# Kernel tuning notes

Measured on AMD Instinct MI355X. Metric: run time of the kernel, lower is better.

The kernel has to match this reference:

```python
import jax, jax.numpy as jnp
import numpy as np

V, D = 1_000_000, 128
N0, N1, N2 = 1_048_576, 131_072, 16_384
E0, E1, EP = 1_048_576, 131_072, 16_384


def setup_inputs() -> dict:
    key = jax.random.key(0)
    ks = jax.random.split(key, 20)
    inp = {
        'emb': jax.random.normal(ks[0], (V, D), jnp.float32) * 0.1,
        'bias': jnp.zeros((V, 1), jnp.float32),
        'nids': jax.random.randint(ks[1], (N0,), 0, V),
        'src0': jax.random.randint(ks[2], (E0,), 0, N0),
        'dst0': jax.random.randint(ks[3], (E0,), 0, N1),
        'w0': jax.random.uniform(ks[4], (E0,), jnp.float32),
        'src1': jax.random.randint(ks[5], (E1,), 0, N1),
        'dst1': jax.random.randint(ks[6], (E1,), 0, N2),
        'w1': jax.random.uniform(ks[7], (E1,), jnp.float32),
        'pos_src': jax.random.randint(ks[8], (EP,), 0, N2),
        'pos_dst': jax.random.randint(ks[9], (EP,), 0, N2),
        'neg_src': jax.random.randint(ks[10], (EP,), 0, N2),
        'neg_dst': jax.random.randint(ks[11], (EP,), 0, N2),
        'Q0w': jax.random.normal(ks[12], (D, D), jnp.float32) / np.sqrt(D),
        'Q0b': jnp.zeros((D,), jnp.float32),
        'W0w': jax.random.normal(ks[13], (2 * D, D), jnp.float32) / np.sqrt(2 * D),
        'W0b': jnp.zeros((D,), jnp.float32),
        'Q1w': jax.random.normal(ks[14], (D, D), jnp.float32) / np.sqrt(D),
        'Q1b': jnp.zeros((D,), jnp.float32),
        'W1w': jax.random.normal(ks[15], (2 * D, D), jnp.float32) / np.sqrt(2 * D),
        'W1b': jnp.zeros((D,), jnp.float32),
    }
    return inp


def _sage_conv(h_src, h_dst, src, dst, w, Qw, Qb, Ww, Wb, n_dst):
    # n = relu(Q h_src); m = sum_e w_e * n[src_e] per dst; ws = sum_e w_e per dst
    n = jax.nn.relu(h_src @ Qw + Qb)                                   # [N_src, H]
    m = jax.ops.segment_sum(n[src] * w[:, None], dst, num_segments=n_dst)
    ws = jnp.clip(jax.ops.segment_sum(w, dst, num_segments=n_dst), 1.0, None)[:, None]
    z = jax.nn.relu(jnp.concatenate([m / ws, h_dst], axis=1) @ Ww + Wb)
    zn = jnp.linalg.norm(z, axis=1, keepdims=True)
    return z / jnp.where(zn == 0, 1.0, zn)


def _pair_score(h, bias_nid, src, dst):
    # u_dot_v + bias_src + bias_dst  -> [E, 1]
    s = jnp.sum(h[src] * h[dst], axis=1, keepdims=True)
    return s + bias_nid[src] + bias_nid[dst]


def reference(emb, bias, nids, src0, dst0, w0, src1, dst1, w1,
              pos_src, pos_dst, neg_src, neg_dst,
              Q0w, Q0b, W0w, W0b, Q1w, Q1b, W1w, W1b):
    h = emb[nids]                                                      # [N0, D]
    h1 = _sage_conv(h, h[:N1], src0, dst0, w0, Q0w, Q0b, W0w, W0b, N1)  # [N1, D]
    h2 = _sage_conv(h1, h1[:N2], src1, dst1, w1, Q1w, Q1b, W1w, W1b, N2)  # [N2, D]
    h_item = emb[nids[:N2]] + h2                                       # [N2, D]
    bias_nid = bias[nids[:N2]]                                         # [N2, 1]
    pos = _pair_score(h_item, bias_nid, pos_src, pos_dst)
    neg = _pair_score(h_item, bias_nid, neg_src, neg_dst)
    return jax.nn.relu(neg - pos + 1.0)                                # [EP, 1]
```

## Files before the change

### kernel.cpp

```cpp
#include <hip/hip_runtime.h>
#include <stdint.h>

#define V_SZ   1000000
#define N0_SZ  1048576
#define N1_SZ  131072
#define N2_SZ  16384
#define E0_SZ  1048576
#define E1_SZ  131072
#define EP_SZ  16384

typedef short bf16x8 __attribute__((ext_vector_type(8)));
typedef float f32x4  __attribute__((ext_vector_type(4)));

__device__ __forceinline__ unsigned short f2bf(float f) {
  union { float f; unsigned u; } v; v.f = f;
  unsigned r = v.u + 0x7FFFu + ((v.u >> 16) & 1u);
  return (unsigned short)(r >> 16);
}
__device__ __forceinline__ float bf2f(unsigned short h) {
  union { unsigned u; float f; } v; v.u = ((unsigned)h) << 16;
  return v.f;
}
__device__ __forceinline__ unsigned pack2bf(float a, float b) {
  return ((unsigned)f2bf(b) << 16) | (unsigned)f2bf(a);
}

__global__ __launch_bounds__(256) void prepw_all_k(
    const float* __restrict__ Q0w, const float* __restrict__ W0w,
    const float* __restrict__ Q1w, const float* __restrict__ W1w,
    unsigned short* __restrict__ Q0T, unsigned short* __restrict__ W0T,
    unsigned short* __restrict__ Q1T, unsigned short* __restrict__ W1T) {
  int t = blockIdx.x * 256 + threadIdx.x;
  const float* W; unsigned short* WT; int K; int base;
  if (t < 16384)      { W = Q0w; WT = Q0T; K = 128; base = 0; }
  else if (t < 49152) { W = W0w; WT = W0T; K = 256; base = 16384; }
  else if (t < 65536) { W = Q1w; WT = Q1T; K = 128; base = 49152; }
  else                { W = W1w; WT = W1T; K = 256; base = 65536; }
  int u = t - base;
  int n = u & 127, k = u >> 7;
  WT[(size_t)n * K + k] = f2bf(W[u]);
}

__global__ __launch_bounds__(256) void hist_all_k(const int* __restrict__ dst0,
                                                  const int* __restrict__ dst1,
                                                  int* __restrict__ counts) {
  int e = blockIdx.x * 256 + threadIdx.x;
  if (e < E0_SZ) atomicAdd(&counts[dst0[e]], 1);
  else if (e < E0_SZ + E1_SZ) atomicAdd(&counts[N1_SZ + dst1[e - E0_SZ]], 1);
}

__global__ __launch_bounds__(256) void scan_bsums_k(const int* __restrict__ counts,
                                                    int* __restrict__ bsums) {
  __shared__ int red[256];
  int base = blockIdx.x * 1024, t = threadIdx.x;
  int s = 0;
  #pragma unroll
  for (int i = 0; i < 4; i++) s += counts[base + t * 4 + i];
  red[t] = s;
  __syncthreads();
  for (int st = 128; st > 0; st >>= 1) {
    if (t < st) red[t] += red[t + st];
    __syncthreads();
  }
  if (t == 0) bsums[blockIdx.x] = red[0];
}

__global__ __launch_bounds__(256) void scan_top2_k(int* __restrict__ bsums,
                                                   int* __restrict__ offs0_last,
                                                   int* __restrict__ offs1_last) {
  __shared__ int lds[256];
  int b = blockIdx.x, t = threadIdx.x;
  int nb = (b == 0) ? 128 : 16;
  int off = (b == 0) ? 0 : 128;
  int v = (t < nb) ? bsums[off + t] : 0;
  lds[t] = v;
  __syncthreads();
  for (int st = 1; st < 256; st <<= 1) {
    int x = (t >= st) ? lds[t - st] : 0;
    __syncthreads();
    lds[t] += x;
    __syncthreads();
  }
  if (t < nb) bsums[off + t] = lds[t] - v;
  if (t == nb - 1) *((b == 0) ? offs0_last : offs1_last) = lds[t];
}

__global__ __launch_bounds__(256) void scan_final_k(const int* __restrict__ counts,
                                                    const int* __restrict__ bsums,
                                                    int* __restrict__ offs0,
                                                    int* __restrict__ offs1) {
  __shared__ int tsum[256];
  int b = blockIdx.x, t = threadIdx.x;
  int base = b * 1024;
  int v0 = counts[base + t * 4 + 0], v1 = counts[base + t * 4 + 1];
  int v2 = counts[base + t * 4 + 2], v3 = counts[base + t * 4 + 3];
  int s = v0 + v1 + v2 + v3;
  tsum[t] = s;
  __syncthreads();
  for (int st = 1; st < 256; st <<= 1) {
    int x = (t >= st) ? tsum[t - st] : 0;
    __syncthreads();
    tsum[t] += x;
    __syncthreads();
  }
  int pre = bsums[b] + tsum[t] - s;
  int* op = (b < 128) ? (offs0 + base) : (offs1 + base - N1_SZ);
  op[t * 4 + 0] = pre;
  op[t * 4 + 1] = pre + v0;
  op[t * 4 + 2] = pre + v0 + v1;
  op[t * 4 + 3] = pre + v0 + v1 + v2;
}

__global__ __launch_bounds__(256) void scatter_all_k(
    const int* __restrict__ src0, const int* __restrict__ dst0, const float* __restrict__ w0,
    const int* __restrict__ src1, const int* __restrict__ dst1, const float* __restrict__ w1,
    const int* __restrict__ offs0, const int* __restrict__ offs1,
    int* __restrict__ cursor,
    int2* __restrict__ esw0, int2* __restrict__ esw1) {
  int e = blockIdx.x * 256 + threadIdx.x;
  if (e < E0_SZ) {
    int d = dst0[e];
    int p = offs0[d] + atomicAdd(&cursor[d], 1);
    esw0[p] = make_int2(src0[e], __float_as_int(w0[e]));
  } else if (e < E0_SZ + E1_SZ) {
    int ee = e - E0_SZ;
    int d = dst1[ee];
    int p = offs1[d] + atomicAdd(&cursor[N1_SZ + d], 1);
    esw1[p] = make_int2(src1[ee], __float_as_int(w1[ee]));
  }
}

#define AM_GATHER 0
#define AM_BF16   1
#define EPI_BF16        0
#define EPI_NORM        1
#define EPI_NORM_ADDEMB 2

template <int KCHUNKS, int AM0, int AM1, int EPI>
__global__ __launch_bounds__(256) void gemm_k(const void* __restrict__ asrc0,
                                              const void* __restrict__ asrc1,
                                              const int* __restrict__ ids,
                                              const unsigned short* __restrict__ BT,
                                              const float* __restrict__ biasv,
                                              void* __restrict__ outp,
                                              const float* __restrict__ emb) {
  __shared__ unsigned short lA[64][136];
  __shared__ unsigned short lB[128][136];
  const int tid = threadIdx.x;
  const int lane = tid & 63;
  const int wid = tid >> 6;
  const int rowbase = blockIdx.x * 64;
  const int Ktot = KCHUNKS * 128;

  f32x4 acc[8];
  #pragma unroll
  for (int i = 0; i < 8; i++) acc[i] = (f32x4){0.f, 0.f, 0.f, 0.f};

  for (int c = 0; c < KCHUNKS; ++c) {
    if (c) __syncthreads();
    const int am = (c == 0) ? AM0 : AM1;
    const void* asrc = (c == 0) ? asrc0 : asrc1;
    if (am == AM_GATHER) {
      const float* fsrc = (const float*)asrc;
      #pragma unroll
      for (int i = 0; i < 8; i++) {
        int f = i * 256 + tid;
        int r = f >> 5, c4 = f & 31;
        const float* rp = fsrc + (size_t)ids[rowbase + r] * 128;
        float4 v = *(const float4*)(rp + c4 * 4);
        uint2 pk;
        pk.x = pack2bf(v.x, v.y);
        pk.y = pack2bf(v.z, v.w);
        *(uint2*)(&lA[r][c4 * 4]) = pk;
      }
    } else {
      const unsigned short* bsrc = (const unsigned short*)asrc;
      #pragma unroll
      for (int i = 0; i < 4; i++) {
        int f = i * 256 + tid;
        int r = f >> 4, c8 = f & 15;
        uint4 v = *(const uint4*)(bsrc + (size_t)(rowbase + r) * 128 + c8 * 8);
        *(uint4*)(&lA[r][c8 * 8]) = v;
      }
    }
    {
      const unsigned short* bp = BT + c * 128;
      #pragma unroll
      for (int i = 0; i < 8; i++) {
        int f = i * 256 + tid;
        int n = f >> 4, c8 = f & 15;
        uint4 v = *(const uint4*)(bp + (size_t)n * Ktot + c8 * 8);
        *(uint4*)(&lB[n][c8 * 8]) = v;
      }
    }
    __syncthreads();

    const int mr = wid * 16 + (lane & 15);
    const int kq = (lane >> 4) * 8;
    #pragma unroll
    for (int kk = 0; kk < 128; kk += 32) {
      bf16x8 af = *(const bf16x8*)(&lA[mr][kk + kq]);
      #pragma unroll
      for (int nt = 0; nt < 8; ++nt) {
        bf16x8 bfr = *(const bf16x8*)(&lB[nt * 16 + (lane & 15)][kk + kq]);
        acc[nt] = __builtin_amdgcn_mfma_f32_16x16x32_bf16(af, bfr, acc[nt], 0, 0, 0);
      }
    }
  }

  const int crow = wid * 16 + ((lane >> 4) << 2);
  float vreg[8][4];
  #pragma unroll
  for (int nt = 0; nt < 8; ++nt) {
    int col = nt * 16 + (lane & 15);
    float b = biasv[col];
    #pragma unroll
    for (int r = 0; r < 4; ++r) {
      float v = acc[nt][r] + b;
      vreg[nt][r] = v > 0.f ? v : 0.f;
    }
  }
  if (EPI == EPI_BF16) {
    unsigned short* op = (unsigned short*)outp;
    #pragma unroll
    for (int nt = 0; nt < 8; ++nt) {
      int col = nt * 16 + (lane & 15);
      #pragma unroll
      for (int r = 0; r < 4; ++r)
        op[(size_t)(rowbase + crow + r) * 128 + col] = f2bf(vreg[nt][r]);
    }
  } else {
    float ss[4] = {0.f, 0.f, 0.f, 0.f};
    #pragma unroll
    for (int nt = 0; nt < 8; ++nt)
      #pragma unroll
      for (int r = 0; r < 4; ++r) ss[r] += vreg[nt][r] * vreg[nt][r];
    #pragma unroll
    for (int r = 0; r < 4; ++r) {
      ss[r] += __shfl_xor(ss[r], 1);
      ss[r] += __shfl_xor(ss[r], 2);
      ss[r] += __shfl_xor(ss[r], 4);
      ss[r] += __shfl_xor(ss[r], 8);
    }
    float sc[4];
    #pragma unroll
    for (int r = 0; r < 4; ++r) sc[r] = ss[r] > 0.f ? rsqrtf(ss[r]) : 1.0f;
    if (EPI == EPI_NORM) {
      unsigned short* op = (unsigned short*)outp;
      #pragma unroll
      for (int nt = 0; nt < 8; ++nt) {
        int col = nt * 16 + (lane & 15);
        #pragma unroll
        for (int r = 0; r < 4; ++r)
          op[(size_t)(rowbase + crow + r) * 128 + col] = f2bf(vreg[nt][r] * sc[r]);
      }
    } else {
      float* op = (float*)outp;
      #pragma unroll
      for (int nt = 0; nt < 8; ++nt) {
        int col = nt * 16 + (lane & 15);
        #pragma unroll
        for (int r = 0; r < 4; ++r) {
          int row = rowbase + crow + r;
          op[(size_t)row * 128 + col] =
              vreg[nt][r] * sc[r] + emb[(size_t)ids[row] * 128 + col];
        }
      }
    }
  }
}

template <int LAYER>
__global__ __launch_bounds__(256) void qagg_k(
    const float* __restrict__ embf,
    const unsigned short* __restrict__ hsrc,
    const int* __restrict__ nids,
    const int* __restrict__ offs,
    const int2* __restrict__ esw,
    const unsigned short* __restrict__ BT,
    const float* __restrict__ biasv,
    unsigned short* __restrict__ aout) {
  __shared__ unsigned short lA[64][136];
  __shared__ unsigned short lB[128][136];
  __shared__ float lw[64];
  __shared__ int loffs[65];
  const int tid = threadIdx.x;
  const int lane = tid & 63;
  const int wid = tid >> 6;
  const int d0 = blockIdx.x * 64;

  #pragma unroll
  for (int i = 0; i < 8; i++) {
    int f = i * 256 + tid;
    int n = f >> 4, c8 = f & 15;
    uint4 v = *(const uint4*)(BT + (size_t)n * 128 + c8 * 8);
    *(uint4*)(&lB[n][c8 * 8]) = v;
  }
  if (tid < 65) loffs[tid] = offs[d0 + tid];
  const int ebeg = offs[d0];
  const int eend = offs[d0 + 64];

  const int mr = wid * 16 + (lane & 15);
  const int kq = (lane >> 4) * 8;
  const int crow = wid * 16 + ((lane >> 4) << 2);

  float bv[8];
  #pragma unroll
  for (int nt = 0; nt < 8; ++nt) bv[nt] = biasv[nt * 16 + (lane & 15)];

  float accD[16][2];
  float wsum[16];
  #pragma unroll
  for (int i = 0; i < 16; ++i) { accD[i][0] = 0.f; accD[i][1] = 0.f; wsum[i] = 0.f; }

  for (int base = ebeg; base < eend; base += 64) {
    const int nslots = min(64, eend - base);
    if (tid < 64) lw[tid] = (tid < nslots) ? __int_as_float(esw[base + tid].y) : 0.f;
    if (LAYER == 0) {
      #pragma unroll
      for (int i = 0; i < 8; i++) {
        int f = i * 256 + tid;
        int r = f >> 5, c4 = f & 31;
        if (r < nslots) {
          int s = esw[base + r].x;
          const float* rp = embf + (size_t)nids[s] * 128;
          float4 v = *(const float4*)(rp + c4 * 4);
          uint2 pk;
          pk.x = pack2bf(v.x, v.y);
          pk.y = pack2bf(v.z, v.w);
          *(uint2*)(&lA[r][c4 * 4]) = pk;
        }
      }
    } else {
      #pragma unroll
      for (int i = 0; i < 4; i++) {
        int f = i * 256 + tid;
        int r = f >> 4, c8 = f & 15;
        if (r < nslots) {
          int s = esw[base + r].x;
          uint4 v = *(const uint4*)(hsrc + (size_t)s * 128 + c8 * 8);
          *(uint4*)(&lA[r][c8 * 8]) = v;
        }
      }
    }
    __syncthreads();

    f32x4 acc[8];
    #pragma unroll
    for (int i = 0; i < 8; i++) acc[i] = (f32x4){0.f, 0.f, 0.f, 0.f};
    #pragma unroll
    for (int kk = 0; kk < 128; kk += 32) {
      bf16x8 af = *(const bf16x8*)(&lA[mr][kk + kq]);
      #pragma unroll
      for (int nt = 0; nt < 8; ++nt) {
        bf16x8 bfr = *(const bf16x8*)(&lB[nt * 16 + (lane & 15)][kk + kq]);
        acc[nt] = __builtin_amdgcn_mfma_f32_16x16x32_bf16(af, bfr, acc[nt], 0, 0, 0);
      }
    }
    #pragma unroll
    for (int nt = 0; nt < 8; ++nt) {
      int col = nt * 16 + (lane & 15);
      #pragma unroll
      for (int r = 0; r < 4; ++r) {
        float v = acc[nt][r] + bv[nt];
        lA[crow + r][col] = f2bf(v > 0.f ? v : 0.f);
      }
    }
    __syncthreads();

    #pragma unroll
    for (int dd = 0; dd < 16; ++dd) {
      const int d = wid * 16 + dd;
      int rb = loffs[d] - base;     rb = rb > 0 ? rb : 0;
      int re = loffs[d + 1] - base; re = re < nslots ? re : nslots;
      for (int r = rb; r < re; ++r) {
        float w = lw[r];
        unsigned u = *(const unsigned*)(&lA[r][lane * 2]);
        accD[dd][0] += w * bf2f((unsigned short)(u & 0xffffu));
        accD[dd][1] += w * bf2f((unsigned short)(u >> 16));
        wsum[dd] += w;
      }
    }
    __syncthreads();
  }

  #pragma unroll
  for (int dd = 0; dd < 16; ++dd) {
    const int d = d0 + wid * 16 + dd;
    float inv = 1.0f / fmaxf(wsum[dd], 1.0f);
    unsigned o = pack2bf(accD[dd][0] * inv, accD[dd][1] * inv);
    *(unsigned*)(aout + (size_t)d * 128 + lane * 2) = o;
  }
}

__global__ __launch_bounds__(256) void score_k(const float* __restrict__ hitem,
                                               const float* __restrict__ bias,
                                               const int* __restrict__ nids,
                                               const int* __restrict__ ps,
                                               const int* __restrict__ pd,
                                               const int* __restrict__ ns,
                                               const int* __restrict__ nd,
                                               float* __restrict__ out) {
  int wid = threadIdx.x >> 6, lane = threadIdx.x & 63;
  int e = blockIdx.x * 4 + wid;
  if (e >= EP_SZ) return;
  int a = ps[e], b = pd[e], c = ns[e], d = nd[e];
  float2 va = ((const float2*)(hitem + (size_t)a * 128))[lane];
  float2 vb = ((const float2*)(hitem + (size_t)b * 128))[lane];
  float2 vc = ((const float2*)(hitem + (size_t)c * 128))[lane];
  float2 vd = ((const float2*)(hitem + (size_t)d * 128))[lane];
  float dp = va.x * vb.x + va.y * vb.y;
  float dn = vc.x * vd.x + vc.y * vd.y;
  #pragma unroll
  for (int m = 1; m < 64; m <<= 1) {
    dp += __shfl_xor(dp, m);
    dn += __shfl_xor(dn, m);
  }
  if (lane == 0) {
    float sp = dp + bias[nids[a]] + bias[nids[b]];
    float sn = dn + bias[nids[c]] + bias[nids[d]];
    out[e] = fmaxf(sn - sp + 1.0f, 0.0f);
  }
}

extern "C" void kernel_launch(void* const* d_in, const int* in_sizes, int n_in,
                              void* d_out, int out_size, void* d_ws, size_t ws_size,
                              hipStream_t stream) {
  const float* emb  = (const float*)d_in[0];
  const float* bias = (const float*)d_in[1];
  const int* nids   = (const int*)d_in[2];
  const int* src0   = (const int*)d_in[3];
  const int* dst0   = (const int*)d_in[4];
  const float* w0   = (const float*)d_in[5];
  const int* src1   = (const int*)d_in[6];
  const int* dst1   = (const int*)d_in[7];
  const float* w1   = (const float*)d_in[8];
  const int* pos_src = (const int*)d_in[9];
  const int* pos_dst = (const int*)d_in[10];
  const int* neg_src = (const int*)d_in[11];
  const int* neg_dst = (const int*)d_in[12];
  const float* Q0w = (const float*)d_in[13];
  const float* Q0b = (const float*)d_in[14];
  const float* W0w = (const float*)d_in[15];
  const float* W0b = (const float*)d_in[16];
  const float* Q1w = (const float*)d_in[17];
  const float* Q1b = (const float*)d_in[18];
  const float* W1w = (const float*)d_in[19];
  const float* W1b = (const float*)d_in[20];
  float* out = (float*)d_out;

  char* ws = (char*)d_ws;
  size_t p = 0;
  auto carve = [&](size_t sz) { void* r = ws + p; p = (p + sz + 255) & ~(size_t)255; return r; };

  unsigned short* a0    = (unsigned short*)carve((size_t)N1_SZ * 128 * 2);
  unsigned short* h1    = (unsigned short*)carve((size_t)N1_SZ * 128 * 2);
  unsigned short* a1    = (unsigned short*)carve((size_t)N2_SZ * 128 * 2);
  float*          hitem = (float*)carve((size_t)N2_SZ * 128 * 4);
  unsigned short* Q0T = (unsigned short*)carve(128 * 128 * 2);
  unsigned short* W0T = (unsigned short*)carve(256 * 128 * 2);
  unsigned short* Q1T = (unsigned short*)carve(128 * 128 * 2);
  unsigned short* W1T = (unsigned short*)carve(256 * 128 * 2);
  int* cnt_all = (int*)carve((size_t)(N1_SZ + N2_SZ) * 2 * 4);
  int* counts  = cnt_all;
  int* cursor  = cnt_all + (N1_SZ + N2_SZ);
  int*  offs0 = (int*)carve((N1_SZ + 1) * 4);
  int*  offs1 = (int*)carve((N2_SZ + 1) * 4);
  int2* esw0  = (int2*)carve((size_t)E0_SZ * 8);
  int2* esw1  = (int2*)carve((size_t)E1_SZ * 8);
  int*  bsums = (int*)carve(160 * 4);
  (void)ws_size; (void)in_sizes; (void)n_in; (void)out_size;

  hipMemsetAsync(cnt_all, 0, (size_t)(N1_SZ + N2_SZ) * 2 * 4, stream);

  prepw_all_k<<<384, 256, 0, stream>>>(Q0w, W0w, Q1w, W1w, Q0T, W0T, Q1T, W1T);

  hist_all_k<<<(E0_SZ + E1_SZ) / 256, 256, 0, stream>>>(dst0, dst1, counts);
  scan_bsums_k<<<(N1_SZ + N2_SZ) / 1024, 256, 0, stream>>>(counts, bsums);
  scan_top2_k<<<2, 256, 0, stream>>>(bsums, offs0 + N1_SZ, offs1 + N2_SZ);
  scan_final_k<<<(N1_SZ + N2_SZ) / 1024, 256, 0, stream>>>(counts, bsums, offs0, offs1);
  scatter_all_k<<<(E0_SZ + E1_SZ) / 256, 256, 0, stream>>>(
      src0, dst0, w0, src1, dst1, w1, offs0, offs1, cursor, esw0, esw1);

  qagg_k<0><<<N1_SZ / 64, 256, 0, stream>>>(emb, nullptr, nids, offs0, esw0,
                                            Q0T, Q0b, a0);
  gemm_k<2, AM_BF16, AM_GATHER, EPI_NORM>
      <<<N1_SZ / 64, 256, 0, stream>>>(a0, emb, nids, W0T, W0b, h1, nullptr);
  qagg_k<1><<<N2_SZ / 64, 256, 0, stream>>>(nullptr, h1, nullptr, offs1, esw1,
                                            Q1T, Q1b, a1);
  gemm_k<2, AM_BF16, AM_BF16, EPI_NORM_ADDEMB>
      <<<N2_SZ / 64, 256, 0, stream>>>(a1, h1, nids, W1T, W1b, hitem, emb);

  score_k<<<EP_SZ / 4, 256, 0, stream>>>(hitem, bias, nids, pos_src, pos_dst,
                                         neg_src, neg_dst, out);
}
```

Before: 1.197 ms.

## Parallelize neighbor aggregation over edge chunks with segmented atomic accumulation

Replaces the per-destination-block aggregation kernel, whose per-block work varies with the edges landing in that block, with an edge-chunk kernel. Each block takes exactly 64 sorted edges, runs the Q transform, then does a segmented per-destination reduction, writing interior segments directly and boundary segments with float atomics into fp32 buffers. The weight-sum normalization moves into the following GEMM's A-load. This evens out load per block but adds fp32 atomics, larger fp32 intermediates, an extra memset of the aggregation buffers and an edst array write.

After: 981.3 us. 1.22x faster.

```diff
diff --git a/kernel.cpp b/kernel.cpp
--- a/kernel.cpp
+++ b/kernel.cpp
@@ -116,22 +116,26 @@
     const int* __restrict__ src1, const int* __restrict__ dst1, const float* __restrict__ w1,
     const int* __restrict__ offs0, const int* __restrict__ offs1,
     int* __restrict__ cursor,
-    int2* __restrict__ esw0, int2* __restrict__ esw1) {
+    int2* __restrict__ esw0, int* __restrict__ edst0,
+    int2* __restrict__ esw1, int* __restrict__ edst1) {
   int e = blockIdx.x * 256 + threadIdx.x;
   if (e < E0_SZ) {
     int d = dst0[e];
     int p = offs0[d] + atomicAdd(&cursor[d], 1);
     esw0[p] = make_int2(src0[e], __float_as_int(w0[e]));
+    edst0[p] = d;
   } else if (e < E0_SZ + E1_SZ) {
     int ee = e - E0_SZ;
     int d = dst1[ee];
     int p = offs1[d] + atomicAdd(&cursor[N1_SZ + d], 1);
     esw1[p] = make_int2(src1[ee], __float_as_int(w1[ee]));
+    edst1[p] = d;
   }
 }
 
 #define AM_GATHER 0
 #define AM_BF16   1
+#define AM_F32DIV 2
 #define EPI_BF16        0
 #define EPI_NORM        1
 #define EPI_NORM_ADDEMB 2
@@ -143,7 +147,8 @@
                                               const unsigned short* __restrict__ BT,
                                               const float* __restrict__ biasv,
                                               void* __restrict__ outp,
-                                              const float* __restrict__ emb) {
+                                              const float* __restrict__ emb,
+                                              const float* __restrict__ wsumv) {
   __shared__ unsigned short lA[64][136];
   __shared__ unsigned short lB[128][136];
   const int tid = threadIdx.x;
@@ -173,6 +178,21 @@
         pk.y = pack2bf(v.z, v.w);
         *(uint2*)(&lA[r][c4 * 4]) = pk;
       }
+    } else if (am == AM_F32DIV) {
+      const float* fsrc = (const float*)asrc;
+      #pragma unroll
+      for (int i = 0; i < 8; i++) {
+        int f = i * 256 + tid;
+        int r = f >> 5, c4 = f & 31;
+        int row = rowbase + r;
+        float inv = 1.0f / fmaxf(wsumv[row], 1.0f);
+        const float* rp = fsrc + (size_t)row * 128;
+        float4 v = *(const float4*)(rp + c4 * 4);
+        uint2 pk;
+        pk.x = pack2bf(v.x * inv, v.y * inv);
+        pk.y = pack2bf(v.z * inv, v.w * inv);
+        *(uint2*)(&lA[r][c4 * 4]) = pk;
+      }
     } else {
       const unsigned short* bsrc = (const unsigned short*)asrc;
       #pragma unroll
@@ -271,125 +291,128 @@
 }
 
 template <int LAYER>
-__global__ __launch_bounds__(256) void qagg_k(
+__global__ __launch_bounds__(256) void eqagg_k(
     const float* __restrict__ embf,
     const unsigned short* __restrict__ hsrc,
     const int* __restrict__ nids,
-    const int* __restrict__ offs,
     const int2* __restrict__ esw,
+    const int* __restrict__ edst,
     const unsigned short* __restrict__ BT,
     const float* __restrict__ biasv,
-    unsigned short* __restrict__ aout) {
+    float* __restrict__ aoutf,
+    float* __restrict__ wsumf) {
+  constexpr int ETOT = (LAYER == 0) ? E0_SZ : E1_SZ;
   __shared__ unsigned short lA[64][136];
   __shared__ unsigned short lB[128][136];
   __shared__ float lw[64];
-  __shared__ int loffs[65];
+  __shared__ int ldst[64];
   const int tid = threadIdx.x;
   const int lane = tid & 63;
   const int wid = tid >> 6;
-  const int d0 = blockIdx.x * 64;
+  const int base0 = blockIdx.x * 64;
 
   #pragma unroll
   for (int i = 0; i < 8; i++) {
     int f = i * 256 + tid;
     int n = f >> 4, c8 = f & 15;
-    uint4 v = *(const uint4*)(BT + (size_t)n * 128 + c8 * 8);
-    *(uint4*)(&lB[n][c8 * 8]) = v;
-  }
-  if (tid < 65) loffs[tid] = offs[d0 + tid];
-  const int ebeg = offs[d0];
-  const int eend = offs[d0 + 64];
+    *(uint4*)(&lB[n][c8 * 8]) = *(const uint4*)(BT + (size_t)n * 128 + c8 * 8);
+  }
+  if (tid < 64) {
+    int2 sw = esw[base0 + tid];
+    lw[tid] = __int_as_float(sw.y);
+    ldst[tid] = edst[base0 + tid];
+  }
+  if (LAYER == 0) {
+    #pragma unroll
+    for (int i = 0; i < 8; i++) {
+      int f = i * 256 + tid;
+      int r = f >> 5, c4 = f & 31;
+      int s = esw[base0 + r].x;
+      const float* rp = embf + (size_t)nids[s] * 128;
+      float4 v = *(const float4*)(rp + c4 * 4);
+      uint2 pk;
+      pk.x = pack2bf(v.x, v.y);
+      pk.y = pack2bf(v.z, v.w);
+      *(uint2*)(&lA[r][c4 * 4]) = pk;
+    }
+  } else {
+    #pragma unroll
+    for (int i = 0; i < 4; i++) {
+      int f = i * 256 + tid;
+      int r = f >> 4, c8 = f & 15;
+      int s = esw[base0 + r].x;
+      *(uint4*)(&lA[r][c8 * 8]) = *(const uint4*)(hsrc + (size_t)s * 128 + c8 * 8);
+    }
+  }
+  __syncthreads();
 
   const int mr = wid * 16 + (lane & 15);
   const int kq = (lane >> 4) * 8;
+  f32x4 acc[8];
+  #pragma unroll
+  for (int i = 0; i < 8; i++) acc[i] = (f32x4){0.f, 0.f, 0.f, 0.f};
+  #pragma unroll
+  for (int kk = 0; kk < 128; kk += 32) {
+    bf16x8 af = *(const bf16x8*)(&lA[mr][kk + kq]);
+    #pragma unroll
+    for (int nt = 0; nt < 8; ++nt) {
+      bf16x8 bfr = *(const bf16x8*)(&lB[nt * 16 + (lane & 15)][kk + kq]);
+      acc[nt] = __builtin_amdgcn_mfma_f32_16x16x32_bf16(af, bfr, acc[nt], 0, 0, 0);
+    }
+  }
   const int crow = wid * 16 + ((lane >> 4) << 2);
-
-  float bv[8];
-  #pragma unroll
-  for (int nt = 0; nt < 8; ++nt) bv[nt] = biasv[nt * 16 + (lane & 15)];
-
-  float accD[16][2];
-  float wsum[16];
-  #pragma unroll
-  for (int i = 0; i < 16; ++i) { accD[i][0] = 0.f; accD[i][1] = 0.f; wsum[i] = 0.f; }
-
-  for (int base = ebeg; base < eend; base += 64) {
-    const int nslots = min(64, eend - base);
-    if (tid < 64) lw[tid] = (tid < nslots) ? __int_as_float(esw[base + tid].y) : 0.f;
-    if (LAYER == 0) {
-      #pragma unroll
-      for (int i = 0; i < 8; i++) {
-        int f = i * 256 + tid;
-        int r = f >> 5, c4 = f & 31;
-        if (r < nslots) {
-          int s = esw[base + r].x;
-          const float* rp = embf + (size_t)nids[s] * 128;
-          float4 v = *(const float4*)(rp + c4 * 4);
-          uint2 pk;
-          pk.x = pack2bf(v.x, v.y);
-          pk.y = pack2bf(v.z, v.w);
-          *(uint2*)(&lA[r][c4 * 4]) = pk;
-        }
-      }
+  #pragma unroll
+  for (int nt = 0; nt < 8; ++nt) {
+    int col = nt * 16 + (lane & 15);
+    float b = biasv[col];
+    #pragma unroll
+    for (int r = 0; r < 4; ++r) {
+      float v = acc[nt][r] + b;
+      lA[crow + r][col] = f2bf(v > 0.f ? v : 0.f);
+    }
+  }
+
+  const int r0 = wid * 16;
+  const int prevd = (wid > 0) ? ldst[r0 - 1]
+                              : (base0 > 0 ? edst[base0 - 1] : -1);
+  const int nextd = (wid < 3) ? ldst[r0 + 16]
+                              : (base0 + 64 < ETOT ? edst[base0 + 64] : -1);
+  float ax = 0.f, ay = 0.f, wa = 0.f;
+  int cur = ldst[r0];
+  int rstart = 0;
+  #pragma unroll
+  for (int rr = 0; rr < 16; ++rr) {
+    int d = ldst[r0 + rr];
+    if (d != cur) {
+      bool interior = (rstart > 0 || prevd != cur);
+      float* rowp = aoutf + (size_t)cur * 128 + lane * 2;
+      if (interior) {
+        rowp[0] = ax; rowp[1] = ay;
+        if (lane == 0) wsumf[cur] = wa;
+      } else {
+        atomicAdd(rowp, ax); atomicAdd(rowp + 1, ay);
+        if (lane == 0) atomicAdd(&wsumf[cur], wa);
+      }
+      ax = ay = wa = 0.f;
+      cur = d;
+      rstart = rr;
+    }
+    float w = lw[r0 + rr];
+    unsigned u = *(const unsigned*)(&lA[r0 + rr][lane * 2]);
+    ax += w * bf2f((unsigned short)(u & 0xffffu));
+    ay += w * bf2f((unsigned short)(u >> 16));
+    wa += w;
+  }
+  {
+    bool interior = (rstart > 0 || prevd != cur) && (nextd != cur);
+    float* rowp = aoutf + (size_t)cur * 128 + lane * 2;
+    if (interior) {
+      rowp[0] = ax; rowp[1] = ay;
+      if (lane == 0) wsumf[cur] = wa;
     } else {
-      #pragma unroll
-      for (int i = 0; i < 4; i++) {
-        int f = i * 256 + tid;
-        int r = f >> 4, c8 = f & 15;
-        if (r < nslots) {
-          int s = esw[base + r].x;
-          uint4 v = *(const uint4*)(hsrc + (size_t)s * 128 + c8 * 8);
-          *(uint4*)(&lA[r][c8 * 8]) = v;
-        }
-      }
-    }
-    __syncthreads();
-
-    f32x4 acc[8];
-    #pragma unroll
-    for (int i = 0; i < 8; i++) acc[i] = (f32x4){0.f, 0.f, 0.f, 0.f};
-    #pragma unroll
-    for (int kk = 0; kk < 128; kk += 32) {
-      bf16x8 af = *(const bf16x8*)(&lA[mr][kk + kq]);
-      #pragma unroll
-      for (int nt = 0; nt < 8; ++nt) {
-        bf16x8 bfr = *(const bf16x8*)(&lB[nt * 16 + (lane & 15)][kk + kq]);
-        acc[nt] = __builtin_amdgcn_mfma_f32_16x16x32_bf16(af, bfr, acc[nt], 0, 0, 0);
-      }
-    }
-    #pragma unroll
-    for (int nt = 0; nt < 8; ++nt) {
-      int col = nt * 16 + (lane & 15);
-      #pragma unroll
-      for (int r = 0; r < 4; ++r) {
-        float v = acc[nt][r] + bv[nt];
-        lA[crow + r][col] = f2bf(v > 0.f ? v : 0.f);
-      }
-    }
-    __syncthreads();
-
-    #pragma unroll
-    for (int dd = 0; dd < 16; ++dd) {
-      const int d = wid * 16 + dd;
-      int rb = loffs[d] - base;     rb = rb > 0 ? rb : 0;
-      int re = loffs[d + 1] - base; re = re < nslots ? re : nslots;
-      for (int r = rb; r < re; ++r) {
-        float w = lw[r];
-        unsigned u = *(const unsigned*)(&lA[r][lane * 2]);
-        accD[dd][0] += w * bf2f((unsigned short)(u & 0xffffu));
-        accD[dd][1] += w * bf2f((unsigned short)(u >> 16));
-        wsum[dd] += w;
-      }
-    }
-    __syncthreads();
-  }
-
-  #pragma unroll
-  for (int dd = 0; dd < 16; ++dd) {
-    const int d = d0 + wid * 16 + dd;
-    float inv = 1.0f / fmaxf(wsum[dd], 1.0f);
-    unsigned o = pack2bf(accD[dd][0] * inv, accD[dd][1] * inv);
-    *(unsigned*)(aout + (size_t)d * 128 + lane * 2) = o;
+      atomicAdd(rowp, ax); atomicAdd(rowp + 1, ay);
+      if (lane == 0) atomicAdd(&wsumf[cur], wa);
+    }
   }
 }
 
@@ -453,25 +476,30 @@
   size_t p = 0;
   auto carve = [&](size_t sz) { void* r = ws + p; p = (p + sz + 255) & ~(size_t)255; return r; };
 
-  unsigned short* a0    = (unsigned short*)carve((size_t)N1_SZ * 128 * 2);
+  float* a0f   = (float*)carve((size_t)N1_SZ * 128 * 4);
+  float* wsum0 = (float*)carve((size_t)N1_SZ * 4);
+  float* a1f   = (float*)carve((size_t)N2_SZ * 128 * 4);
+  float* wsum1 = (float*)carve((size_t)N2_SZ * 4);
+  int* cnt_all = (int*)carve((size_t)(N1_SZ + N2_SZ) * 2 * 4);
+  size_t zlen  = p;
+  int* counts  = cnt_all;
+  int* cursor  = cnt_all + (N1_SZ + N2_SZ);
   unsigned short* h1    = (unsigned short*)carve((size_t)N1_SZ * 128 * 2);
-  unsigned short* a1    = (unsigned short*)carve((size_t)N2_SZ * 128 * 2);
   float*          hitem = (float*)carve((size_t)N2_SZ * 128 * 4);
   unsigned short* Q0T = (unsigned short*)carve(128 * 128 * 2);
   unsigned short* W0T = (unsigned short*)carve(256 * 128 * 2);
   unsigned short* Q1T = (unsigned short*)carve(128 * 128 * 2);
   unsigned short* W1T = (unsigned short*)carve(256 * 128 * 2);
-  int* cnt_all = (int*)carve((size_t)(N1_SZ + N2_SZ) * 2 * 4);
-  int* counts  = cnt_all;
-  int* cursor  = cnt_all + (N1_SZ + N2_SZ);
   int*  offs0 = (int*)carve((N1_SZ + 1) * 4);
   int*  offs1 = (int*)carve((N2_SZ + 1) * 4);
   int2* esw0  = (int2*)carve((size_t)E0_SZ * 8);
+  int*  edst0 = (int*)carve((size_t)E0_SZ * 4);
   int2* esw1  = (int2*)carve((size_t)E1_SZ * 8);
+  int*  edst1 = (int*)carve((size_t)E1_SZ * 4);
   int*  bsums = (int*)carve(160 * 4);
   (void)ws_size; (void)in_sizes; (void)n_in; (void)out_size;
 
-  hipMemsetAsync(cnt_all, 0, (size_t)(N1_SZ + N2_SZ) * 2 * 4, stream);
+  hipMemsetAsync(ws, 0, zlen, stream);
 
   prepw_all_k<<<384, 256, 0, stream>>>(Q0w, W0w, Q1w, W1w, Q0T, W0T, Q1T, W1T);
 
@@ -480,16 +508,17 @@
   scan_top2_k<<<2, 256, 0, stream>>>(bsums, offs0 + N1_SZ, offs1 + N2_SZ);
   scan_final_k<<<(N1_SZ + N2_SZ) / 1024, 256, 0, stream>>>(counts, bsums, offs0, offs1);
   scatter_all_k<<<(E0_SZ + E1_SZ) / 256, 256, 0, stream>>>(
-      src0, dst0, w0, src1, dst1, w1, offs0, offs1, cursor, esw0, esw1);
-
-  qagg_k<0><<<N1_SZ / 64, 256, 0, stream>>>(emb, nullptr, nids, offs0, esw0,
-                                            Q0T, Q0b, a0);
-  gemm_k<2, AM_BF16, AM_GATHER, EPI_NORM>
-      <<<N1_SZ / 64, 256, 0, stream>>>(a0, emb, nids, W0T, W0b, h1, nullptr);
-  qagg_k<1><<<N2_SZ / 64, 256, 0, stream>>>(nullptr, h1, nullptr, offs1, esw1,
-                                            Q1T, Q1b, a1);
-  gemm_k<2, AM_BF16, AM_BF16, EPI_NORM_ADDEMB>
-      <<<N2_SZ / 64, 256, 0, stream>>>(a1, h1, nids, W1T, W1b, hitem, emb);
+      src0, dst0, w0, src1, dst1, w1, offs0, offs1, cursor,
+      esw0, edst0, esw1, edst1);
+
+  eqagg_k<0><<<E0_SZ / 64, 256, 0, stream>>>(emb, nullptr, nids, esw0, edst0,
+                                             Q0T, Q0b, a0f, wsum0);
+  gemm_k<2, AM_F32DIV, AM_GATHER, EPI_NORM>
+      <<<N1_SZ / 64, 256, 0, stream>>>(a0f, emb, nids, W0T, W0b, h1, nullptr, wsum0);
+  eqagg_k<1><<<E1_SZ / 64, 256, 0, stream>>>(nullptr, h1, nullptr, esw1, edst1,
+                                             Q1T, Q1b, a1f, wsum1);
+  gemm_k<2, AM_F32DIV, AM_BF16, EPI_NORM_ADDEMB>
+      <<<N2_SZ / 64, 256, 0, stream>>>(a1f, h1, nids, W1T, W1b, hitem, emb, wsum1);
 
   score_k<<<EP_SZ / 4, 256, 0, stream>>>(hitem, bias, nids, pos_src, pos_dst,
                                          neg_src, neg_dst, out);
```
